# Kernel optimization log

Measured on AMD Instinct MI355X. Metric: run time of the kernel, lower is better.

Reference implementation:

```python
import jax, jax.numpy as jnp
import numpy as np

B, DIM, N_SIDE = 32, 256, 32
HEADS, DIM_K, DIM_U = 4, 16, 1
DIM_V = 64  # dim_out // heads
EPS = 1e-5

def _rel_pos_idx(n):
    # matches calc_rel_pos: meshgrid(ij) -> (N,2), pairwise diff + (n-1)
    i = np.arange(n)
    pos = np.stack(np.meshgrid(i, i, indexing='ij'), 0).reshape(2, -1).T  # (N, 2)
    rel = pos[None, :] - pos[:, None] + (n - 1)                            # (N, N, 2)
    return rel[..., 0], rel[..., 1]

def _bn(t, gamma, beta):
    # BatchNorm2d in training mode: batch stats over (B, H, W), biased var
    mu = t.mean(axis=(0, 2, 3), keepdims=True)
    var = t.var(axis=(0, 2, 3), keepdims=True)
    xhat = (t - mu) * jax.lax.rsqrt(var + EPS)
    return xhat * gamma[None, :, None, None] + beta[None, :, None, None]

def setup_inputs() -> dict:
    key = jax.random.key(0)
    ks = jax.random.split(key, 5)
    rl = 2 * N_SIDE - 1
    return {
        'x': jax.random.normal(ks[0], (B, DIM, N_SIDE, N_SIDE), jnp.float32),
        'w_q': jax.random.normal(ks[1], (DIM_K * HEADS, DIM), jnp.float32) * 0.05,
        'w_k': jax.random.normal(ks[2], (DIM_K * DIM_U, DIM), jnp.float32) * 0.05,
        'w_v': jax.random.normal(ks[3], (DIM_V * DIM_U, DIM), jnp.float32) * 0.05,
        'gamma_q': jnp.ones((DIM_K * HEADS,), jnp.float32),
        'beta_q': jnp.zeros((DIM_K * HEADS,), jnp.float32),
        'gamma_v': jnp.ones((DIM_V * DIM_U,), jnp.float32),
        'beta_v': jnp.zeros((DIM_V * DIM_U,), jnp.float32),
        'rel_pos_emb': jax.random.normal(ks[4], (rl, rl, DIM_K, DIM_U), jnp.float32),
    }

def reference(x, w_q, w_k, w_v, gamma_q, beta_q, gamma_v, beta_v, rel_pos_emb):
    b, c, hh, ww = x.shape
    n = hh * ww
    # 1x1 convs as channel contractions
    q = _bn(jnp.einsum('oc,bchw->bohw', w_q, x), gamma_q, beta_q)
    k = jnp.einsum('oc,bchw->bohw', w_k, x)
    v = _bn(jnp.einsum('oc,bchw->bohw', w_v, x), gamma_v, beta_v)
    q = q.reshape(b, HEADS, DIM_K, n)   # b h k n
    k = k.reshape(b, DIM_U, DIM_K, n)   # b u k m
    v = v.reshape(b, DIM_U, DIM_V, n)   # b u v m
    k = jax.nn.softmax(k, axis=-1)
    # content lambda
    lam_c = jnp.einsum('bukm,buvm->bkv', k, v)
    Yc = jnp.einsum('bhkn,bkv->bhvn', q, lam_c)
    # positional lambda via relative-position embedding gather
    ni, mi = _rel_pos_idx(N_SIDE)
    emb = rel_pos_emb[ni, mi]                      # (n, n, k, u)
    lam_p = jnp.einsum('nmku,buvm->bnkv', emb, v)  # dominant compute
    Yp = jnp.einsum('bhkn,bnkv->bhvn', q, lam_p)
    Y = Yc + Yp                                    # b h v n
    return Y.reshape(b, HEADS * DIM_V, hh, ww)
```

## Files before the change

### kernel.cpp

```cpp
#include <hip/hip_runtime.h>

using u16 = unsigned short;
using u32 = unsigned int;

typedef __attribute__((ext_vector_type(4))) float f32x4;
typedef __attribute__((ext_vector_type(4))) u16 u16x4;
typedef __attribute__((ext_vector_type(8))) u16 u16x8;
typedef __attribute__((ext_vector_type(8))) short s16x8;

__device__ __forceinline__ u16 f2bf(float f) {
  u32 x = __builtin_bit_cast(u32, f);
  x += 0x7fffu + ((x >> 16) & 1u);
  return (u16)(x >> 16);
}
__device__ __forceinline__ float bf2f(u16 u) {
  u32 x = ((u32)u) << 16;
  return __builtin_bit_cast(float, x);
}

__global__ __launch_bounds__(256) void k_prep(
    const float* __restrict__ wq, const float* __restrict__ wk,
    const float* __restrict__ wv, const float* __restrict__ R,
    u16* __restrict__ Wb, u16* __restrict__ APre)
{
  const int blk = blockIdx.x;
  const int t = threadIdx.x;
  if (blk < 144) {
    const int o = blk;
    const float* src = (o < 64) ? (wq + o * 256)
                     : (o < 80) ? (wk + (o - 64) * 256)
                                : (wv + (o - 80) * 256);
    Wb[o * 256 + t] = f2bf(src[t]);
  } else {
    const int di = blk - 144;
    const int w = t >> 6, l = t & 63;
    const int g = l >> 4, k = l & 15;
    for (int j1 = w; j1 < 32; j1 += 4) {
      u16x8 o8;
#pragma unroll
      for (int e = 0; e < 8; ++e) {
        int dj = 8 * g + e - j1 + 31;
        o8[e] = f2bf(R[(di * 63 + dj) * 16 + k]);
      }
      *(u16x8*)(APre + ((di * 32 + j1) * 64 + l) * 8) = o8;
    }
  }
}

__global__ __launch_bounds__(256) void k_proj(
    const float* __restrict__ x, const u16* __restrict__ Wb,
    float* __restrict__ q_raw, float* __restrict__ k_raw,
    float* __restrict__ v_raw)
{
  __shared__ u16 XLb[64][264];
  const int b  = blockIdx.x >> 4;
  const int p0 = (blockIdx.x & 15) * 64;
  const int t  = threadIdx.x;

  {
    const int p4 = (t & 15) * 4;
    const int cb = (t >> 4);
#pragma unroll
    for (int i = 0; i < 8; ++i) {
      const int c = 2 * (i * 16 + cb);
      f32x4 xa = *(const f32x4*)&x[(b * 256 + c) * 1024 + p0 + p4];
      f32x4 xb = *(const f32x4*)&x[(b * 256 + c + 1) * 1024 + p0 + p4];
#pragma unroll
      for (int j = 0; j < 4; ++j) {
        u32 pk = (u32)f2bf(xa[j]) | ((u32)f2bf(xb[j]) << 16);
        *(u32*)&XLb[p4 + j][c] = pk;
      }
    }
  }
  __syncthreads();

  const int w  = t >> 6;
  const int l  = t & 63;
  const int g  = l >> 4;
  const int cc = l & 15;
  const int p  = p0 + w * 16 + cc;

  f32x4 acc[9];
  const f32x4 fz = {0.f, 0.f, 0.f, 0.f};
#pragma unroll
  for (int mt = 0; mt < 9; ++mt) acc[mt] = fz;

#pragma unroll
  for (int ko = 0; ko < 8; ++ko) {
    s16x8 bfr = *(const s16x8*)&XLb[w * 16 + cc][ko * 32 + g * 8];
#pragma unroll
    for (int mt = 0; mt < 9; ++mt) {
      s16x8 afr = *(const s16x8*)&Wb[(mt * 16 + cc) * 256 + ko * 32 + g * 8];
      acc[mt] = __builtin_amdgcn_mfma_f32_16x16x32_bf16(afr, bfr, acc[mt], 0, 0, 0);
    }
  }

#pragma unroll
  for (int mt = 0; mt < 9; ++mt) {
#pragma unroll
    for (int r = 0; r < 4; ++r) {
      const int o = mt * 16 + 4 * g + r;
      const float val = acc[mt][r];
      if (mt < 4)       q_raw[(b * 64 + o) * 1024 + p] = val;
      else if (mt == 4) k_raw[(b * 16 + (o - 64)) * 1024 + p] = val;
      else              v_raw[(b * 64 + (o - 80)) * 1024 + p] = val;
    }
  }
}

__global__ __launch_bounds__(256) void k_stats(
    const float* __restrict__ q_raw, const float* __restrict__ v_raw,
    const float* __restrict__ k_raw,
    float* __restrict__ qs1, float* __restrict__ qs2,
    float* __restrict__ vs1, float* __restrict__ vs2,
    float* __restrict__ kmax, float* __restrict__ kinv)
{
  const int blk = blockIdx.x;
  const int t = threadIdx.x;
  const int w = t >> 6, lane = t & 63;
  if (blk < 128) {
    const float* src = (blk < 64) ? q_raw : v_raw;
    float* s1g = (blk < 64) ? qs1 : vs1;
    float* s2g = (blk < 64) ? qs2 : vs2;
    const int rv0 = (blk & 63) * 32;
    for (int rr = w; rr < 32; rr += 4) {
      const int rv = rv0 + rr;
      const float* row = src + rv * 1024;
      float s1 = 0.f, s2 = 0.f;
      for (int m = lane; m < 1024; m += 64) { float xx = row[m]; s1 += xx; s2 += xx * xx; }
#pragma unroll
      for (int off = 32; off; off >>= 1) { s1 += __shfl_down(s1, off); s2 += __shfl_down(s2, off); }
      if (lane == 0) { atomicAdd(&s1g[rv & 63], s1); atomicAdd(&s2g[rv & 63], s2); }
    }
  } else {
    const int j = blk - 128;
    for (int rr = w * 2; rr < w * 2 + 2; ++rr) {
      const int row = j * 8 + rr;
      const float* kr = k_raw + row * 1024;
      float mx = -3.0e38f;
      for (int m = lane; m < 1024; m += 64) mx = fmaxf(mx, kr[m]);
#pragma unroll
      for (int off = 32; off; off >>= 1) mx = fmaxf(mx, __shfl_xor(mx, off));
      float s = 0.f;
      for (int m = lane; m < 1024; m += 64) s += __expf(kr[m] - mx);
#pragma unroll
      for (int off = 32; off; off >>= 1) s += __shfl_xor(s, off);
      if (lane == 0) { kmax[row] = mx; kinv[row] = 1.0f / s; }
    }
  }
}

__global__ __launch_bounds__(256) void k_norm(
    const float* __restrict__ v_raw,
    const float* __restrict__ vs1, const float* __restrict__ vs2,
    const float* __restrict__ gv, const float* __restrict__ bv,
    u16* __restrict__ vn, u16* __restrict__ vnF)
{
  const int b  = blockIdx.x >> 5;
  const int i2 = blockIdx.x & 31;
  const int t  = threadIdx.x;
  const int tt = t >> 6, l = t & 63;
  const int v  = tt * 16 + (l & 15);
  const int m8 = i2 * 32 + (l >> 4) * 8;
  const float invN = 1.0f / 32768.0f;
  const float mu = vs1[v] * invN;
  const float var = vs2[v] * invN - mu * mu;
  const float rs = rsqrtf(var + 1e-5f);
  const float sc = rs * gv[v];
  const float bi = bv[v] - mu * sc;
  const float* src = v_raw + (b * 64 + v) * 1024 + m8;
  f32x4 a = *(const f32x4*)src;
  f32x4 c = *(const f32x4*)(src + 4);
  u16x8 o8;
#pragma unroll
  for (int j = 0; j < 4; ++j) o8[j] = f2bf(a[j] * sc + bi);
#pragma unroll
  for (int j = 0; j < 4; ++j) o8[4 + j] = f2bf(c[j] * sc + bi);
  *(u16x8*)&vnF[((b * 32 + i2) * 4 + tt) * 512 + l * 8] = o8;
  *(u16x8*)&vn[(b * 64 + v) * 1024 + m8] = o8;
}

__global__ __launch_bounds__(256) void k_lamc(
    const float* __restrict__ k_raw, const float* __restrict__ kmax,
    const float* __restrict__ kinv, const u16* __restrict__ vn,
    float* __restrict__ lam_c)
{
  __shared__ float KE[16][132];
  const int b  = blockIdx.x >> 3;
  const int m0 = (blockIdx.x & 7) * 128;
  const int t  = threadIdx.x;
  {
    const int kc = t >> 4, mm = (t & 15) * 8;
    const int row = b * 16 + kc;
    const float* kr = k_raw + row * 1024 + m0 + mm;
    const float mx = kmax[row], iv = kinv[row];
#pragma unroll
    for (int j = 0; j < 8; ++j) KE[kc][mm + j] = __expf(kr[j] - mx) * iv;
  }
  __syncthreads();
  const int kc = t & 15, vg = t >> 4;
  const u16* vb = vn + b * 65536 + m0;
  float acc[4] = {0.f, 0.f, 0.f, 0.f};
  for (int m4 = 0; m4 < 128; m4 += 4) {
    f32x4 ke = *(const f32x4*)&KE[kc][m4];
#pragma unroll
    for (int j = 0; j < 4; ++j) {
      u16x4 vv = *(const u16x4*)&vb[(vg * 4 + j) * 1024 + m4];
      acc[j] += ke[0] * bf2f(vv[0]) + ke[1] * bf2f(vv[1])
              + ke[2] * bf2f(vv[2]) + ke[3] * bf2f(vv[3]);
    }
  }
#pragma unroll
  for (int j = 0; j < 4; ++j)
    atomicAdd(&lam_c[(b * 16 + kc) * 64 + vg * 4 + j], acc[j]);
}

__global__ __launch_bounds__(256, 3) void k_main(
    const u16* __restrict__ APre, const u16* __restrict__ vnF,
    const float* __restrict__ q_raw, const float* __restrict__ lam_c,
    const float* __restrict__ qs1, const float* __restrict__ qs2,
    const float* __restrict__ gq, const float* __restrict__ bq,
    float* __restrict__ out)
{
  __shared__ alignas(16) u16 BB[2][4096];
  __shared__ float QL[64][17];
  __shared__ float YL[256][18];
  const int bid  = blockIdx.x;
  const int xcd  = bid & 7;
  const int s    = bid >> 3;
  const int b    = xcd * 4 + (s & 3);
  const int rest = s >> 2;
  const int i1   = rest >> 1;
  const int half = rest & 1;
  const int t  = threadIdx.x;
  const int w  = t >> 6;
  const int l  = t & 63;
  const int g  = l >> 4;
  const int c  = l & 15;
  const int j1base = half * 16 + w * 4;

  const u16* vF = vnF + b * 65536;

  f32x4 acc[4][4];
  const f32x4 fz = {0.f, 0.f, 0.f, 0.f};
#pragma unroll
  for (int nn = 0; nn < 4; ++nn)
#pragma unroll
    for (int tt = 0; tt < 4; ++tt) acc[nn][tt] = fz;

  {
    const int o = t >> 2, ns = (t & 3) * 4;
    const float invN = 1.0f / 32768.0f;
    const float mu = qs1[o] * invN;
    const float var = qs2[o] * invN - mu * mu;
    const float rs = rsqrtf(var + 1e-5f);
    const float sc = rs * gq[o];
    const float bi = bq[o] - mu * sc;
    f32x4 qa = *(const f32x4*)&q_raw[(b * 64 + o) * 1024 + i1 * 32 + half * 16 + ns];
#pragma unroll
    for (int j = 0; j < 4; ++j) QL[o][ns + j] = qa[j] * sc + bi;
  }
  {
    u16x8 b0 = *(const u16x8*)(vF + t * 8);
    u16x8 b1 = *(const u16x8*)(vF + 2048 + t * 8);
    *(u16x8*)&BB[0][t * 8] = b0;
    *(u16x8*)&BB[0][2048 + t * 8] = b1;
  }
  __syncthreads();

  s16x8 afrA[8], afrB[8];
  {
#pragma unroll
    for (int sub = 0; sub < 2; ++sub) {
      const u16* ab = APre + (((sub - i1 + 31) * 32) + j1base) * 512 + l * 8;
#pragma unroll
      for (int nn = 0; nn < 4; ++nn)
        afrA[sub * 4 + nn] = *(const s16x8*)(ab + nn * 512);
    }
  }

  auto body = [&](int p, int cur, s16x8 (&AC)[8], s16x8 (&AN)[8]) {
    u16x8 bn0, bn1;
    const bool pf = (p < 15);
    if (pf) {
      bn0 = *(const u16x8*)(vF + (p + 1) * 4096 + t * 8);
      bn1 = *(const u16x8*)(vF + (p + 1) * 4096 + 2048 + t * 8);
#pragma unroll
      for (int sub = 0; sub < 2; ++sub) {
        const int i2s = 2 * (p + 1) + sub;
        const u16* anb = APre + (((i2s - i1 + 31) * 32) + j1base) * 512 + l * 8;
#pragma unroll
        for (int nn = 0; nn < 4; ++nn)
          AN[sub * 4 + nn] = *(const s16x8*)(anb + nn * 512);
      }
    }
    s16x8 bfr[8];
#pragma unroll
    for (int sub = 0; sub < 2; ++sub)
#pragma unroll
      for (int tt = 0; tt < 4; ++tt)
        bfr[sub * 4 + tt] = *(const s16x8*)&BB[cur][sub * 2048 + tt * 512 + l * 8];
#pragma unroll
    for (int sub = 0; sub < 2; ++sub)
#pragma unroll
      for (int nn = 0; nn < 4; ++nn)
#pragma unroll
        for (int tt = 0; tt < 4; ++tt)
          acc[nn][tt] = __builtin_amdgcn_mfma_f32_16x16x32_bf16(
              AC[sub * 4 + nn], bfr[sub * 4 + tt], acc[nn][tt], 0, 0, 0);
    if (pf) {
      *(u16x8*)&BB[cur ^ 1][t * 8] = bn0;
      *(u16x8*)&BB[cur ^ 1][2048 + t * 8] = bn1;
    }
    asm volatile("s_waitcnt lgkmcnt(0)" ::: "memory");
    __builtin_amdgcn_sched_barrier(0);
    __builtin_amdgcn_s_barrier();
    __builtin_amdgcn_sched_barrier(0);
  };

  for (int ii = 0; ii < 8; ++ii) {
    body(2 * ii, 0, afrA, afrB);
    body(2 * ii + 1, 1, afrB, afrA);
  }

  {
    const float* lcb = lam_c + b * 1024;
#pragma unroll
    for (int tt = 0; tt < 4; ++tt)
#pragma unroll
      for (int r = 0; r < 4; ++r) {
        const float lv = lcb[(4 * g + r) * 64 + tt * 16 + c];
#pragma unroll
        for (int nn = 0; nn < 4; ++nn) acc[nn][tt][r] += lv;
      }
  }
#pragma unroll
  for (int nn = 0; nn < 4; ++nn) {
    const int j1loc = w * 4 + nn;
#pragma unroll
    for (int h = 0; h < 4; ++h) {
      const float q0 = QL[h * 16 + 4 * g + 0][j1loc];
      const float q1 = QL[h * 16 + 4 * g + 1][j1loc];
      const float q2 = QL[h * 16 + 4 * g + 2][j1loc];
      const float q3 = QL[h * 16 + 4 * g + 3][j1loc];
#pragma unroll
      for (int tt = 0; tt < 4; ++tt) {
        float sY = q0 * acc[nn][tt][0] + q1 * acc[nn][tt][1]
                 + q2 * acc[nn][tt][2] + q3 * acc[nn][tt][3];
        sY += __shfl_xor(sY, 16);
        sY += __shfl_xor(sY, 32);
        if (g == h) YL[h * 64 + tt * 16 + c][j1loc] = sY;
      }
    }
  }
  __syncthreads();
#pragma unroll
  for (int it = 0; it < 4; ++it) {
    const int o  = (t >> 2) + it * 64;
    const int nf = (t & 3) * 4;
    f32x4 v4 = *(const f32x4*)&YL[o][nf];
    *(f32x4*)&out[(b * 256 + o) * 1024 + i1 * 32 + half * 16 + nf] = v4;
  }
}

extern "C" void kernel_launch(void* const* d_in, const int* in_sizes, int n_in,
                              void* d_out, int out_size, void* d_ws, size_t ws_size,
                              hipStream_t stream) {
  const float* x  = (const float*)d_in[0];
  const float* wq = (const float*)d_in[1];
  const float* wk = (const float*)d_in[2];
  const float* wv = (const float*)d_in[3];
  const float* gq = (const float*)d_in[4];
  const float* bq = (const float*)d_in[5];
  const float* gv = (const float*)d_in[6];
  const float* bv = (const float*)d_in[7];
  const float* R  = (const float*)d_in[8];
  float* out = (float*)d_out;

  float* wsf   = (float*)d_ws;
  float* q_raw = wsf;
  float* k_raw = q_raw + 32 * 64 * 1024;
  float* v_raw = k_raw + 32 * 16 * 1024;
  float* lam_c = v_raw + 32 * 64 * 1024;
  float* qs1   = lam_c + 32 * 16 * 64;
  float* qs2   = qs1 + 64;
  float* vs1   = qs2 + 64;
  float* vs2   = vs1 + 64;
  float* kmax  = vs2 + 64;
  float* kinv  = kmax + 512;
  u16*   vn    = (u16*)(kinv + 512);
  u16*   vnF   = vn + 32 * 64 * 1024;
  u16*   APre  = vnF + 32 * 65536;
  u16*   Wb    = APre + 63 * 32 * 512;

  hipMemsetAsync(lam_c, 0, (32 * 16 * 64 + 256) * sizeof(float), stream);
  k_prep<<<207, 256, 0, stream>>>(wq, wk, wv, R, Wb, APre);
  k_proj<<<512, 256, 0, stream>>>(x, Wb, q_raw, k_raw, v_raw);
  k_stats<<<192, 256, 0, stream>>>(q_raw, v_raw, k_raw, qs1, qs2, vs1, vs2, kmax, kinv);
  k_norm<<<1024, 256, 0, stream>>>(v_raw, vs1, vs2, gv, bv, vn, vnF);
  k_lamc<<<256, 256, 0, stream>>>(k_raw, kmax, kinv, vn, lam_c);
  k_main<<<2048, 256, 0, stream>>>(APre, vnF, q_raw, lam_c, qs1, qs2, gq, bq, out);
}
```

Before: 166.5 us.

## Double per-block query tile in k_main to halve B-operand reloads

Each k_main block now covers a full row of 32 query positions (8 per wave) instead of 16, so the grid shrinks from 2048 to 1024 blocks. Each staged V tile in shared memory and each B fragment read then feeds twice as many MFMAs, cutting vnF global traffic and LDS reads per unit of work. The A-fragment loads are split into finer chunks interleaved with the MFMA groups to hide their latency. In exchange the accumulators double to 32 f32x4 per thread and launch bounds drop to 2 blocks per CU, which lowers occupancy, and the shared-memory buffers for Q and Y grow.

Measured after the change: 180.4 us. 8.4% more time.

```diff
diff --git a/kernel.cpp b/kernel.cpp
--- a/kernel.cpp
+++ b/kernel.cpp
@@ -215,7 +215,26 @@
     atomicAdd(&lam_c[(b * 16 + kc) * 64 + vg * 4 + j], acc[j]);
 }
 
-__global__ __launch_bounds__(256, 3) void k_main(
+template <int NNG>
+__device__ __forceinline__ void mfma_chunk(f32x4 (&acc)[8][4],
+                                           const s16x8 (&A)[4],
+                                           const s16x8 (&B)[4])
+{
+#pragma unroll
+  for (int j = 0; j < 4; ++j)
+#pragma unroll
+    for (int tt = 0; tt < 4; ++tt)
+      acc[NNG * 4 + j][tt] = __builtin_amdgcn_mfma_f32_16x16x32_bf16(
+          A[j], B[tt], acc[NNG * 4 + j][tt], 0, 0, 0);
+}
+
+__device__ __forceinline__ void load_a4(s16x8 (&dst)[4], const u16* ab)
+{
+#pragma unroll
+  for (int j = 0; j < 4; ++j) dst[j] = *(const s16x8*)(ab + j * 512);
+}
+
+__global__ __launch_bounds__(256, 2) void k_main(
     const u16* __restrict__ APre, const u16* __restrict__ vnF,
     const float* __restrict__ q_raw, const float* __restrict__ lam_c,
     const float* __restrict__ qs1, const float* __restrict__ qs2,
@@ -223,42 +242,44 @@
     float* __restrict__ out)
 {
   __shared__ alignas(16) u16 BB[2][4096];
-  __shared__ float QL[64][17];
-  __shared__ float YL[256][18];
+  __shared__ float QL[64][33];
+  __shared__ float YL[256][36];
   const int bid  = blockIdx.x;
   const int xcd  = bid & 7;
   const int s    = bid >> 3;
   const int b    = xcd * 4 + (s & 3);
-  const int rest = s >> 2;
-  const int i1   = rest >> 1;
-  const int half = rest & 1;
+  const int i1   = s >> 2;
   const int t  = threadIdx.x;
   const int w  = t >> 6;
   const int l  = t & 63;
   const int g  = l >> 4;
   const int c  = l & 15;
-  const int j1base = half * 16 + w * 4;
+  const int j1base = w * 8;
 
   const u16* vF = vnF + b * 65536;
 
-  f32x4 acc[4][4];
+  f32x4 acc[8][4];
   const f32x4 fz = {0.f, 0.f, 0.f, 0.f};
 #pragma unroll
-  for (int nn = 0; nn < 4; ++nn)
+  for (int nn = 0; nn < 8; ++nn)
 #pragma unroll
     for (int tt = 0; tt < 4; ++tt) acc[nn][tt] = fz;
 
   {
-    const int o = t >> 2, ns = (t & 3) * 4;
+    const int o = t >> 2, ns = (t & 3) * 8;
     const float invN = 1.0f / 32768.0f;
     const float mu = qs1[o] * invN;
     const float var = qs2[o] * invN - mu * mu;
     const float rs = rsqrtf(var + 1e-5f);
     const float sc = rs * gq[o];
     const float bi = bq[o] - mu * sc;
-    f32x4 qa = *(const f32x4*)&q_raw[(b * 64 + o) * 1024 + i1 * 32 + half * 16 + ns];
-#pragma unroll
-    for (int j = 0; j < 4; ++j) QL[o][ns + j] = qa[j] * sc + bi;
+    f32x4 qa = *(const f32x4*)&q_raw[(b * 64 + o) * 1024 + i1 * 32 + ns];
+    f32x4 qb = *(const f32x4*)&q_raw[(b * 64 + o) * 1024 + i1 * 32 + ns + 4];
+#pragma unroll
+    for (int j = 0; j < 4; ++j) {
+      QL[o][ns + j]     = qa[j] * sc + bi;
+      QL[o][ns + 4 + j] = qb[j] * sc + bi;
+    }
   }
   {
     u16x8 b0 = *(const u16x8*)(vF + t * 8);
@@ -266,48 +287,35 @@
     *(u16x8*)&BB[0][t * 8] = b0;
     *(u16x8*)&BB[0][2048 + t * 8] = b1;
   }
+
+  s16x8 afrA[4], afrB[4];
+  load_a4(afrA, APre + ((0 - i1 + 31) * 32 + j1base) * 512 + l * 8);
   __syncthreads();
 
-  s16x8 afrA[8], afrB[8];
-  {
-#pragma unroll
-    for (int sub = 0; sub < 2; ++sub) {
-      const u16* ab = APre + (((sub - i1 + 31) * 32) + j1base) * 512 + l * 8;
-#pragma unroll
-      for (int nn = 0; nn < 4; ++nn)
-        afrA[sub * 4 + nn] = *(const s16x8*)(ab + nn * 512);
-    }
-  }
-
-  auto body = [&](int p, int cur, s16x8 (&AC)[8], s16x8 (&AN)[8]) {
+  for (int p = 0; p < 16; ++p) {
+    const int cur = p & 1;
+    const bool pf = (p < 15);
     u16x8 bn0, bn1;
-    const bool pf = (p < 15);
     if (pf) {
       bn0 = *(const u16x8*)(vF + (p + 1) * 4096 + t * 8);
       bn1 = *(const u16x8*)(vF + (p + 1) * 4096 + 2048 + t * 8);
-#pragma unroll
-      for (int sub = 0; sub < 2; ++sub) {
-        const int i2s = 2 * (p + 1) + sub;
-        const u16* anb = APre + (((i2s - i1 + 31) * 32) + j1base) * 512 + l * 8;
-#pragma unroll
-        for (int nn = 0; nn < 4; ++nn)
-          AN[sub * 4 + nn] = *(const s16x8*)(anb + nn * 512);
-      }
-    }
-    s16x8 bfr[8];
-#pragma unroll
-    for (int sub = 0; sub < 2; ++sub)
-#pragma unroll
-      for (int tt = 0; tt < 4; ++tt)
-        bfr[sub * 4 + tt] = *(const s16x8*)&BB[cur][sub * 2048 + tt * 512 + l * 8];
-#pragma unroll
-    for (int sub = 0; sub < 2; ++sub)
-#pragma unroll
-      for (int nn = 0; nn < 4; ++nn)
-#pragma unroll
-        for (int tt = 0; tt < 4; ++tt)
-          acc[nn][tt] = __builtin_amdgcn_mfma_f32_16x16x32_bf16(
-              AC[sub * 4 + nn], bfr[sub * 4 + tt], acc[nn][tt], 0, 0, 0);
+    }
+    s16x8 bfr[4];
+    load_a4(afrB, APre + ((2 * p + 0 - i1 + 31) * 32 + j1base + 4) * 512 + l * 8);
+#pragma unroll
+    for (int tt = 0; tt < 4; ++tt)
+      bfr[tt] = *(const s16x8*)&BB[cur][tt * 512 + l * 8];
+    mfma_chunk<0>(acc, afrA, bfr);
+    load_a4(afrA, APre + ((2 * p + 1 - i1 + 31) * 32 + j1base) * 512 + l * 8);
+    mfma_chunk<1>(acc, afrB, bfr);
+    load_a4(afrB, APre + ((2 * p + 1 - i1 + 31) * 32 + j1base + 4) * 512 + l * 8);
+#pragma unroll
+    for (int tt = 0; tt < 4; ++tt)
+      bfr[tt] = *(const s16x8*)&BB[cur][2048 + tt * 512 + l * 8];
+    mfma_chunk<0>(acc, afrA, bfr);
+    if (pf)
+      load_a4(afrA, APre + ((2 * p + 2 - i1 + 31) * 32 + j1base) * 512 + l * 8);
+    mfma_chunk<1>(acc, afrB, bfr);
     if (pf) {
       *(u16x8*)&BB[cur ^ 1][t * 8] = bn0;
       *(u16x8*)&BB[cur ^ 1][2048 + t * 8] = bn1;
@@ -316,11 +324,6 @@
     __builtin_amdgcn_sched_barrier(0);
     __builtin_amdgcn_s_barrier();
     __builtin_amdgcn_sched_barrier(0);
-  };
-
-  for (int ii = 0; ii < 8; ++ii) {
-    body(2 * ii, 0, afrA, afrB);
-    body(2 * ii + 1, 1, afrB, afrA);
   }
 
   {
@@ -331,12 +334,12 @@
       for (int r = 0; r < 4; ++r) {
         const float lv = lcb[(4 * g + r) * 64 + tt * 16 + c];
 #pragma unroll
-        for (int nn = 0; nn < 4; ++nn) acc[nn][tt][r] += lv;
+        for (int nn = 0; nn < 8; ++nn) acc[nn][tt][r] += lv;
       }
   }
 #pragma unroll
-  for (int nn = 0; nn < 4; ++nn) {
-    const int j1loc = w * 4 + nn;
+  for (int nn = 0; nn < 8; ++nn) {
+    const int j1loc = w * 8 + nn;
 #pragma unroll
     for (int h = 0; h < 4; ++h) {
       const float q0 = QL[h * 16 + 4 * g + 0][j1loc];
@@ -355,11 +358,11 @@
   }
   __syncthreads();
 #pragma unroll
-  for (int it = 0; it < 4; ++it) {
-    const int o  = (t >> 2) + it * 64;
-    const int nf = (t & 3) * 4;
+  for (int it = 0; it < 8; ++it) {
+    const int o  = (t >> 3) + it * 32;
+    const int nf = (t & 7) * 4;
     f32x4 v4 = *(const f32x4*)&YL[o][nf];
-    *(f32x4*)&out[(b * 256 + o) * 1024 + i1 * 32 + half * 16 + nf] = v4;
+    *(f32x4*)&out[(b * 256 + o) * 1024 + i1 * 32 + nf] = v4;
   }
 }
 
@@ -399,5 +402,5 @@
   k_stats<<<192, 256, 0, stream>>>(q_raw, v_raw, k_raw, qs1, qs2, vs1, vs2, kmax, kinv);
   k_norm<<<1024, 256, 0, stream>>>(v_raw, vs1, vs2, gv, bv, vn, vnF);
   k_lamc<<<256, 256, 0, stream>>>(k_raw, kmax, kinv, vn, lam_c);
-  k_main<<<2048, 256, 0, stream>>>(APre, vnF, q_raw, lam_c, qs1, qs2, gq, bq, out);
-}
+  k_main<<<1024, 256, 0, stream>>>(APre, vnF, q_raw, lam_c, qs1, qs2, gq, bq, out);
+}
```

## Use direct global-to-LDS loads and finer A-fragment prefetch in main kernel

Applied to the files above, without the earlier changes.

Replaces register-staged B-tile copies into shared memory with global_load_lds direct loads, so the data no longer passes through VGPRs. The A-fragment prefetch is split into two half-sized register sets interleaved with the two MFMA sub-steps, cutting register pressure, and launch bounds are raised to allow 4 blocks per CU. The barrier wait now uses a partial vmcnt instead of an lgkmcnt drain. There is a risk that the vmcnt(4) count does not correctly cover the outstanding LDS-direct loads, and the tighter A-prefetch distance may expose more load latency.

After: 165.9 us. No clear change (-0.4%).

```diff
diff --git a/kernel.cpp b/kernel.cpp
--- a/kernel.cpp
+++ b/kernel.cpp
@@ -16,6 +16,12 @@
 __device__ __forceinline__ float bf2f(u16 u) {
   u32 x = ((u32)u) << 16;
   return __builtin_bit_cast(float, x);
+}
+
+__device__ __forceinline__ void glds16(const u16* gsrc, u16* ldst) {
+  __builtin_amdgcn_global_load_lds(
+      (const __attribute__((address_space(1))) unsigned int*)gsrc,
+      (__attribute__((address_space(3))) unsigned int*)ldst, 16, 0, 0);
 }
 
 __global__ __launch_bounds__(256) void k_prep(
@@ -215,7 +221,13 @@
     atomicAdd(&lam_c[(b * 16 + kc) * 64 + vg * 4 + j], acc[j]);
 }
 
-__global__ __launch_bounds__(256, 3) void k_main(
+__device__ __forceinline__ void load_a4(s16x8 (&dst)[4], const u16* ab)
+{
+#pragma unroll
+  for (int j = 0; j < 4; ++j) dst[j] = *(const s16x8*)(ab + j * 512);
+}
+
+__global__ __launch_bounds__(256, 4) void k_main(
     const u16* __restrict__ APre, const u16* __restrict__ vnF,
     const float* __restrict__ q_raw, const float* __restrict__ lam_c,
     const float* __restrict__ qs1, const float* __restrict__ qs2,
@@ -227,9 +239,9 @@
   __shared__ float YL[256][18];
   const int bid  = blockIdx.x;
   const int xcd  = bid & 7;
-  const int s    = bid >> 3;
-  const int b    = xcd * 4 + (s & 3);
-  const int rest = s >> 2;
+  const int sb   = bid >> 3;
+  const int b    = xcd * 4 + (sb & 3);
+  const int rest = sb >> 2;
   const int i1   = rest >> 1;
   const int half = rest & 1;
   const int t  = threadIdx.x;
@@ -261,66 +273,52 @@
     for (int j = 0; j < 4; ++j) QL[o][ns + j] = qa[j] * sc + bi;
   }
   {
-    u16x8 b0 = *(const u16x8*)(vF + t * 8);
-    u16x8 b1 = *(const u16x8*)(vF + 2048 + t * 8);
-    *(u16x8*)&BB[0][t * 8] = b0;
-    *(u16x8*)&BB[0][2048 + t * 8] = b1;
-  }
+    const u16* src = vF + w * 1024 + l * 8;
+    u16* dst = &BB[0][w * 1024];
+    glds16(src, dst);
+    glds16(src + 512, dst + 512);
+  }
+
+  s16x8 afrP[4], afrQ[4];
+  const u16* aB = APre + ((31 - i1) * 32 + j1base) * 512 + l * 8;
+  load_a4(afrP, aB);
   __syncthreads();
 
-  s16x8 afrA[8], afrB[8];
-  {
-#pragma unroll
-    for (int sub = 0; sub < 2; ++sub) {
-      const u16* ab = APre + (((sub - i1 + 31) * 32) + j1base) * 512 + l * 8;
-#pragma unroll
-      for (int nn = 0; nn < 4; ++nn)
-        afrA[sub * 4 + nn] = *(const s16x8*)(ab + nn * 512);
-    }
-  }
-
-  auto body = [&](int p, int cur, s16x8 (&AC)[8], s16x8 (&AN)[8]) {
-    u16x8 bn0, bn1;
+  for (int p = 0; p < 16; ++p) {
+    const int cur = p & 1;
     const bool pf = (p < 15);
     if (pf) {
-      bn0 = *(const u16x8*)(vF + (p + 1) * 4096 + t * 8);
-      bn1 = *(const u16x8*)(vF + (p + 1) * 4096 + 2048 + t * 8);
-#pragma unroll
-      for (int sub = 0; sub < 2; ++sub) {
-        const int i2s = 2 * (p + 1) + sub;
-        const u16* anb = APre + (((i2s - i1 + 31) * 32) + j1base) * 512 + l * 8;
-#pragma unroll
-        for (int nn = 0; nn < 4; ++nn)
-          AN[sub * 4 + nn] = *(const s16x8*)(anb + nn * 512);
-      }
-    }
-    s16x8 bfr[8];
-#pragma unroll
-    for (int sub = 0; sub < 2; ++sub)
+      const u16* src = vF + (p + 1) * 4096 + w * 1024 + l * 8;
+      u16* dst = &BB[cur ^ 1][w * 1024];
+      glds16(src, dst);
+      glds16(src + 512, dst + 512);
+    }
+    __builtin_amdgcn_sched_barrier(0);
+    s16x8 bfr[4];
+#pragma unroll
+    for (int tt = 0; tt < 4; ++tt)
+      bfr[tt] = *(const s16x8*)&BB[cur][tt * 512 + l * 8];
+    load_a4(afrQ, aB + (2 * p + 1) * 16384);
+#pragma unroll
+    for (int nn = 0; nn < 4; ++nn)
 #pragma unroll
       for (int tt = 0; tt < 4; ++tt)
-        bfr[sub * 4 + tt] = *(const s16x8*)&BB[cur][sub * 2048 + tt * 512 + l * 8];
-#pragma unroll
-    for (int sub = 0; sub < 2; ++sub)
-#pragma unroll
-      for (int nn = 0; nn < 4; ++nn)
-#pragma unroll
-        for (int tt = 0; tt < 4; ++tt)
-          acc[nn][tt] = __builtin_amdgcn_mfma_f32_16x16x32_bf16(
-              AC[sub * 4 + nn], bfr[sub * 4 + tt], acc[nn][tt], 0, 0, 0);
-    if (pf) {
-      *(u16x8*)&BB[cur ^ 1][t * 8] = bn0;
-      *(u16x8*)&BB[cur ^ 1][2048 + t * 8] = bn1;
-    }
-    asm volatile("s_waitcnt lgkmcnt(0)" ::: "memory");
+        acc[nn][tt] = __builtin_amdgcn_mfma_f32_16x16x32_bf16(
+            afrP[nn], bfr[tt], acc[nn][tt], 0, 0, 0);
+#pragma unroll
+    for (int tt = 0; tt < 4; ++tt)
+      bfr[tt] = *(const s16x8*)&BB[cur][2048 + tt * 512 + l * 8];
+    if (pf) load_a4(afrP, aB + (2 * p + 2) * 16384);
+#pragma unroll
+    for (int nn = 0; nn < 4; ++nn)
+#pragma unroll
+      for (int tt = 0; tt < 4; ++tt)
+        acc[nn][tt] = __builtin_amdgcn_mfma_f32_16x16x32_bf16(
+            afrQ[nn], bfr[tt], acc[nn][tt], 0, 0, 0);
+    asm volatile("s_waitcnt vmcnt(4)" ::: "memory");
     __builtin_amdgcn_sched_barrier(0);
     __builtin_amdgcn_s_barrier();
     __builtin_amdgcn_sched_barrier(0);
-  };
-
-  for (int ii = 0; ii < 8; ++ii) {
-    body(2 * ii, 0, afrA, afrB);
-    body(2 * ii + 1, 1, afrB, afrA);
   }
 
   {
```
